# Optimization experiments

Measured on AMD Instinct MI355X. Metric: run time of the kernel, lower is better.

The kernel has to match this reference:

```python
import jax, jax.numpy as jnp
import numpy as np

B, GH, GW = 64, 14, 14
H = 512   # features_len == lstm hidden size == lstm_len
E = 512   # embedding_len
A = 512   # attention_len
V = 10000 # wordmap_len
MAXCAP = 50


def setup_inputs() -> dict:
    key = jax.random.key(0)
    ks = jax.random.split(key, 12)
    s = 0.02
    caplens = jax.random.randint(ks[2], (B, 1), 2, MAXCAP + 1, jnp.int32)
    caplens = caplens.at[0, 0].set(MAXCAP)  # ensure max(decode_lengths) == MAXCAP-1 (static T)
    return dict(
        image_features=jax.random.normal(ks[0], (B, GH, GW, H), jnp.float32),
        caps=jax.random.randint(ks[1], (B, MAXCAP), 0, V, jnp.int32),
        caplens=caplens,
        emb_table=jax.random.normal(ks[3], (V, E), jnp.float32) * s,
        W_ih=jax.random.normal(ks[4], (4 * H, E + H), jnp.float32) * s,
        W_hh=jax.random.normal(ks[5], (4 * H, H), jnp.float32) * s,
        b_ih=jnp.zeros((4 * H,), jnp.float32),
        b_hh=jnp.zeros((4 * H,), jnp.float32),
        W_enc=jax.random.normal(ks[6], (A, H), jnp.float32) * s,
        b_enc=jnp.zeros((A,), jnp.float32),
        W_dec=jax.random.normal(ks[7], (A, H), jnp.float32) * s,
        b_dec=jnp.zeros((A,), jnp.float32),
        W_full=jax.random.normal(ks[8], (1, A), jnp.float32) * s,
        b_full=jnp.zeros((1,), jnp.float32),
        W_score=jax.random.normal(ks[9], (V, H), jnp.float32) * s,
        b_score=jnp.zeros((V,), jnp.float32),
    )


def _forward(image_features, emb_table, W_ih, W_hh, b_ih, b_hh,
             W_enc, b_enc, W_dec, b_dec, W_full, b_full, W_score, b_score,
             caps, caplens):
    Bsz = image_features.shape[0]
    feats = image_features.reshape(Bsz, -1, image_features.shape[-1])  # (B, P, H)
    cl = caplens[:, 0]
    sort_ind = jnp.argsort(-cl)                      # descending sort by caption length
    cl = cl[sort_ind]
    feats = feats[sort_ind]
    caps_s = caps[sort_ind]
    decode_lengths = cl - 1
    T = caps.shape[1] - 1                            # static; setup guarantees max(decode_lengths)==T
    emb = emb_table[caps_s]                          # (B, MAXCAP, E)
    enc_att = jnp.einsum('bph,ah->bpa', feats, W_enc) + b_enc  # precomputed encoder attention proj
    mask = jnp.arange(T)[None, :] < decode_lengths[:, None]    # (B, T): row active at step t

    h0 = jnp.zeros((Bsz, feats.shape[-1]), feats.dtype)
    c0 = jnp.zeros_like(h0)

    def step(carry, xs):
        h, c = carry
        emb_t, m_t = xs                              # (B,E), (B,)
        # attention (show-attend-tell style)
        att2 = h @ W_dec.T + b_dec                   # (B, A)
        e = jnp.einsum('bpa,a->bp', jax.nn.relu(enc_att + att2[:, None, :]), W_full[0]) + b_full[0]
        alpha = jax.nn.softmax(e, axis=-1)           # (B, P)
        ctx = jnp.einsum('bp,bph->bh', alpha, feats) # (B, H)
        # LSTMCell
        x = jnp.concatenate([emb_t, ctx], axis=1)    # (B, E+H)
        gates = x @ W_ih.T + b_ih + h @ W_hh.T + b_hh
        i, f, g, o = jnp.split(gates, 4, axis=1)
        c_new = jax.nn.sigmoid(f) * c + jax.nn.sigmoid(i) * jnp.tanh(g)
        h_new = jax.nn.sigmoid(o) * jnp.tanh(c_new)
        score = h_new @ W_score.T + b_score          # (B, V)
        m = m_t[:, None]
        # rows past their decode length keep stale state and write zeros (matches :k slicing)
        h = jnp.where(m, h_new, h)
        c = jnp.where(m, c_new, c)
        return (h, c), (jnp.where(m, score, jnp.zeros((), score.dtype)),
                        jnp.where(m, alpha, jnp.zeros((), alpha.dtype)))

    (_, _), (scores, weights) = jax.lax.scan(
        step, (h0, c0), (emb[:, :T, :].transpose(1, 0, 2), mask.T))
    scores = scores.transpose(1, 0, 2)   # (B, T, V)
    weights = weights.transpose(1, 0, 2) # (B, T, P)
    return scores, caps_s, decode_lengths, weights, sort_ind


def reference(image_features, caps, caplens, emb_table, W_ih, W_hh, b_ih, b_hh,
              W_enc, b_enc, W_dec, b_dec, W_full, b_full, W_score, b_score):
    return _forward(image_features, emb_table, W_ih, W_hh, b_ih, b_hh,
                    W_enc, b_enc, W_dec, b_dec, W_full, b_full, W_score, b_score,
                    caps, caplens)
```

## Files before the change

kernel.cpp:

```cpp
#include <hip/hip_runtime.h>
#include <math.h>


#define WS_SORT   0
#define WS_DL     64
#define WS_NB     128
#define WS_ROWOFF 192
#define WS_CAPS   256
#define WS_RMAP   3456
#define WS_H      6592
#define WS_C      39360
#define WS_ATT2   72128
#define WS_E      104896
#define WS_Z      117696
#define WS_CTXP   117952
#define WS_PG     249024
#define WS_HALL   2346176
#define WS_ENC    3951808

#define OUT_SCORES 0
#define OUT_CAPS   31360000
#define OUT_DL     31363200
#define OUT_W      31363264
#define OUT_SORT   31977920

#define LSW 196

__device__ __forceinline__ float sigm(float x) { return 1.f / (1.f + expf(-x)); }

__device__ __forceinline__ float4 f4add(float4 a, float4 b) {
  return make_float4(a.x + b.x, a.y + b.y, a.z + b.z, a.w + b.w);
}

__device__ __forceinline__ int swz128(int m) { return (m >> 3) * 12 + (m & 7); }

__device__ __forceinline__ void stage128_strided(const float* __restrict__ src, int row0, int ld, int k0,
                                                 float* __restrict__ dst, int tid, int nrows_valid) {
#pragma unroll
  for (int i = 0; i < 2; ++i) {
    int lin = tid + 256 * i;
    int m = lin >> 2, kf = lin & 3;
    float4 v = make_float4(0.f, 0.f, 0.f, 0.f);
    if (m < nrows_valid) v = *(const float4*)(src + (long)(row0 + m) * ld + k0 + kf * 4);
    int mc = swz128(m);
    dst[(kf * 4 + 0) * LSW + mc] = v.x;
    dst[(kf * 4 + 1) * LSW + mc] = v.y;
    dst[(kf * 4 + 2) * LSW + mc] = v.z;
    dst[(kf * 4 + 3) * LSW + mc] = v.w;
  }
}

__device__ __forceinline__ void stage128_gather(const float* __restrict__ src, const int* __restrict__ bases,
                                                int k0, float* __restrict__ dst, int tid) {
#pragma unroll
  for (int i = 0; i < 2; ++i) {
    int lin = tid + 256 * i;
    int m = lin >> 2, kf = lin & 3;
    float4 v = *(const float4*)(src + bases[m] + k0 + kf * 4);
    int mc = swz128(m);
    dst[(kf * 4 + 0) * LSW + mc] = v.x;
    dst[(kf * 4 + 1) * LSW + mc] = v.y;
    dst[(kf * 4 + 2) * LSW + mc] = v.z;
    dst[(kf * 4 + 3) * LSW + mc] = v.w;
  }
}

__device__ __forceinline__ void gemm_acc128(const float* __restrict__ As, const float* __restrict__ Bs,
                                            float acc[8][8], int tx, int ty) {
#pragma unroll
  for (int kk = 0; kk < 16; ++kk) {
    const float4* ar = (const float4*)(As + kk * LSW + tx * 12);
    const float4* br = (const float4*)(Bs + kk * LSW + ty * 12);
    float4 a0 = ar[0], a1 = ar[1];
    float4 b0 = br[0], b1 = br[1];
    float av[8] = {a0.x, a0.y, a0.z, a0.w, a1.x, a1.y, a1.z, a1.w};
    float bv[8] = {b0.x, b0.y, b0.z, b0.w, b1.x, b1.y, b1.z, b1.w};
#pragma unroll
    for (int i = 0; i < 8; ++i)
#pragma unroll
      for (int j = 0; j < 8; ++j)
        acc[i][j] = fmaf(av[i], bv[j], acc[i][j]);
  }
}

__global__ __launch_bounds__(64) void setup_kernel(const int* __restrict__ caps, const int* __restrict__ caplens,
                                                   float* __restrict__ ws, float* __restrict__ out) {
  __shared__ int cl_s[64], so_s[64], dl_s[64], nb_s[49], ro_s[50];
  int i = threadIdx.x;
  cl_s[i] = caplens[i];
  __syncthreads();
  int cli = cl_s[i];
  int r = 0;
  for (int j = 0; j < 64; ++j) {
    int clj = cl_s[j];
    r += (clj > cli) || (clj == cli && j < i);
  }
  so_s[r] = i;
  dl_s[r] = cli - 1;
  __syncthreads();
  int* iws = (int*)ws;
  iws[WS_SORT + i] = so_s[i];
  iws[WS_DL + i] = dl_s[i];
  out[OUT_SORT + i] = (float)so_s[i];
  out[OUT_DL + i] = (float)dl_s[i];
  if (i < 49) {
    int n = 0;
    for (int b = 0; b < 64; ++b) n += (dl_s[b] > i);
    iws[WS_NB + i] = n;
    nb_s[i] = n;
  }
  __syncthreads();
  if (i == 0) {
    int acc = 0;
    for (int t = 0; t < 49; ++t) { ro_s[t] = acc; acc += nb_s[t]; }
    ro_s[49] = acc;
    iws[WS_NB + 49] = acc;
  }
  __syncthreads();
  if (i < 50) iws[WS_ROWOFF + i] = ro_s[i];
  int R = ro_s[49];
  for (int rr = i; rr < 3136; rr += 64) {
    int val = 0;
    if (rr < R) {
      int t = 0;
      while (t < 48 && ro_s[t + 1] <= rr) ++t;
      val = t * 64 + (rr - ro_s[t]);
    }
    iws[WS_RMAP + rr] = val;
  }
  for (int j = i; j < 3200; j += 64) {
    int k = j / 50, jj = j - k * 50;
    int cv = caps[so_s[k] * 50 + jj];
    iws[WS_CAPS + j] = cv;
    out[OUT_CAPS + j] = (float)cv;
  }
}

__global__ void zero_init_kernel(float* __restrict__ out, float* __restrict__ ws, const float* __restrict__ b_dec) {
  const float4 z = make_float4(0.f, 0.f, 0.f, 0.f);
  float4* out4 = (float4*)out;
  float4* ws4 = (float4*)ws;
  const float4* bd4 = (const float4*)b_dec;
  for (long idx = (long)blockIdx.x * 256 + threadIdx.x; idx < 8018240L; idx += (long)gridDim.x * 256) {
    if (idx < 7840000L) {
      out4[idx] = z;
    } else if (idx < 7993664L) {
      out4[7840816L + (idx - 7840000L)] = z;
    } else if (idx < 8010048L) {
      ws4[1648L + (idx - 7993664L)] = z;
    } else {
      long j = idx - 8010048L;
      ws4[18032L + j] = bd4[j & 127];
    }
  }
}

__global__ __launch_bounds__(256) void encatt_kernel(const float* __restrict__ image, const float* __restrict__ W_enc,
                                                     const float* __restrict__ b_enc, float* __restrict__ ws) {
  __shared__ __align__(16) float As[16 * LSW];
  __shared__ __align__(16) float Bs[16 * LSW];
  __shared__ int rb[128];
  int tid = threadIdx.x;
  const int* iws = (const int*)ws;
  int mt = blockIdx.x, nt = blockIdx.y;
  if (tid < 128) {
    int r = mt * 128 + tid;
    int b = r / 196;
    int p = r - b * 196;
    rb[tid] = iws[WS_SORT + b] * 100352 + p * 512;
  }
  float acc[8][8] = {};
  for (int ch = 0; ch < 32; ++ch) {
    __syncthreads();
    stage128_gather(image, rb, ch * 16, As, tid);
    stage128_strided(W_enc, nt * 128, 512, ch * 16, Bs, tid, 128);
    __syncthreads();
    gemm_acc128(As, Bs, acc, tid & 15, tid >> 4);
  }
  int tx = tid & 15, ty = tid >> 4;
  int r0 = mt * 128 + tx * 8;
  int n0 = nt * 128 + ty * 8;
#pragma unroll
  for (int i = 0; i < 8; ++i) {
    float* cp = ws + WS_ENC + (long)(r0 + i) * 512 + n0;
    *(float4*)(cp)     = make_float4(acc[i][0] + b_enc[n0],     acc[i][1] + b_enc[n0 + 1],
                                     acc[i][2] + b_enc[n0 + 2], acc[i][3] + b_enc[n0 + 3]);
    *(float4*)(cp + 4) = make_float4(acc[i][4] + b_enc[n0 + 4], acc[i][5] + b_enc[n0 + 5],
                                     acc[i][6] + b_enc[n0 + 6], acc[i][7] + b_enc[n0 + 7]);
  }
}

__global__ __launch_bounds__(512) void ectx_kernel(float* __restrict__ ws, const float* __restrict__ image,
                                                   const float* __restrict__ W_full, const float* __restrict__ b_full,
                                                   int t) {
  const int* iws = (const int*)ws;
  int b = blockIdx.x;
  if (b >= iws[WS_NB + t]) return;
  int pg = blockIdx.y;
  __shared__ float att2_s[512], wf_s[512], e_s[52];
  int tid = threadIdx.x;
  att2_s[tid] = ws[WS_ATT2 + b * 512 + tid];
  wf_s[tid] = W_full[tid];
  __syncthreads();
  int w = tid >> 6, lane = tid & 63;
  float bf0 = b_full[0];
  for (int idx = w; idx < 49; idx += 8) {
    int p = pg * 49 + idx;
    const float* er = ws + WS_ENC + (long)(b * 196 + p) * 512;
    float acc = 0.f;
#pragma unroll
    for (int a8 = 0; a8 < 8; ++a8) {
      int a = (a8 << 6) + lane;
      float v = er[a] + att2_s[a];
      acc = fmaf(fmaxf(v, 0.f), wf_s[a], acc);
    }
#pragma unroll
    for (int off = 32; off; off >>= 1) acc += __shfl_down(acc, off);
    if (lane == 0) e_s[idx] = expf(acc + bf0);
  }
  __syncthreads();
  if (tid < 49) ws[WS_E + b * 200 + pg * 49 + tid] = e_s[tid];
  if (tid == 0) {
    float zz = 0.f;
    for (int j = 0; j < 49; ++j) zz += e_s[j];
    ws[WS_Z + pg * 64 + b] = zz;
  }
  long sb = (long)iws[WS_SORT + b] * 100352;
  float a0 = 0.f;
  for (int j = 0; j < 49; ++j) {
    a0 = fmaf(e_s[j], image[sb + (long)(pg * 49 + j) * 512 + tid], a0);
  }
  ws[WS_CTXP + pg * 32768 + b * 512 + tid] = a0;
}

__global__ __launch_bounds__(256) void gates_kernel(float* __restrict__ ws, const float* __restrict__ emb,
                                                    const float* __restrict__ W_ih, const float* __restrict__ W_hh,
                                                    int t) {
  __shared__ __align__(16) float As[96 * 68];
  __shared__ __align__(16) float Bs[96 * 68];
  __shared__ int rbe[64];
  __shared__ float rcpz_s[64];
  int tid = threadIdx.x;
  int nt = blockIdx.x;
  int ks = blockIdx.y;
  int* iws = (int*)ws;
  if (tid < 64) {
    rbe[tid] = iws[WS_CAPS + tid * 50 + t] * 512;
    float zz = ws[WS_Z + tid] + ws[WS_Z + 64 + tid] + ws[WS_Z + 128 + tid] + ws[WS_Z + 192 + tid];
    rcpz_s[tid] = 1.f / zz;
  }
  __syncthreads();
#pragma unroll
  for (int c = 0; c < 3; ++c) {
    int k0 = ks * 96 + c * 32;
#pragma unroll
    for (int i = 0; i < 2; ++i) {
      int lin = tid + 256 * i;
      int kf = lin >> 6;
      int m = lin & 63;
      float4 v;
      if (k0 < 512) {
        v = *(const float4*)(emb + (long)rbe[m] + k0 + kf * 4);
      } else if (k0 < 1024) {
        const float* base = ws + WS_CTXP + m * 512 + (k0 - 512) + kf * 4;
        float4 v0 = *(const float4*)(base);
        float4 v1 = *(const float4*)(base + 32768);
        float4 v2 = *(const float4*)(base + 65536);
        float4 v3 = *(const float4*)(base + 98304);
        float rz = rcpz_s[m];
        v = make_float4((v0.x + v1.x + v2.x + v3.x) * rz, (v0.y + v1.y + v2.y + v3.y) * rz,
                        (v0.z + v1.z + v2.z + v3.z) * rz, (v0.w + v1.w + v2.w + v3.w) * rz);
      } else {
        v = *(const float4*)(ws + WS_H + m * 512 + (k0 - 1024) + kf * 4);
      }
      float* da = As + (c * 32 + kf * 4) * 68 + m;
      da[0] = v.x; da[68] = v.y; da[136] = v.z; da[204] = v.w;
      const float* srcB = (k0 < 1024) ? (W_ih + (long)(nt * 64 + m) * 1024 + k0 + kf * 4)
                                      : (W_hh + (long)(nt * 64 + m) * 512 + (k0 - 1024) + kf * 4);
      float4 bv = *(const float4*)srcB;
      float* db = Bs + (c * 32 + kf * 4) * 68 + m;
      db[0] = bv.x; db[68] = bv.y; db[136] = bv.z; db[204] = bv.w;
    }
  }
  __syncthreads();
  int w = tid >> 6, lane = tid & 63;
  int tx = lane & 7, ty = lane >> 3;
  float acc[8][2] = {};
#pragma unroll 8
  for (int kk = 0; kk < 96; ++kk) {
    const float4* ar = (const float4*)(As + kk * 68 + tx * 8);
    float4 a0 = ar[0], a1 = ar[1];
    float2 bv = *(const float2*)(Bs + kk * 68 + w * 16 + ty * 2);
    float av[8] = {a0.x, a0.y, a0.z, a0.w, a1.x, a1.y, a1.z, a1.w};
#pragma unroll
    for (int i = 0; i < 8; ++i) {
      acc[i][0] = fmaf(av[i], bv.x, acc[i][0]);
      acc[i][1] = fmaf(av[i], bv.y, acc[i][1]);
    }
  }
  float* pg = ws + WS_PG + ks * 131072;
  int j0 = nt * 64 + w * 16 + ty * 2;
#pragma unroll
  for (int i = 0; i < 8; ++i) {
    int b = tx * 8 + i;
    *(float2*)(pg + b * 2048 + j0) = make_float2(acc[i][0], acc[i][1]);
  }
}

__global__ __launch_bounds__(512) void lstm_att2_kernel(float* __restrict__ ws, const float* __restrict__ b_ih,
                                                        const float* __restrict__ b_hh, const float* __restrict__ W_dec,
                                                        const float* __restrict__ b_dec, float* __restrict__ out, int t) {
  const int* iws = (const int*)ws;
  int b = blockIdx.x;
  int as = blockIdx.y;
  int hh = threadIdx.x;
  int nb = iws[WS_NB + t];
  __shared__ float h_s[512], red[512];
  float gi = b_ih[hh] + b_hh[hh];
  float gf = b_ih[512 + hh] + b_hh[512 + hh];
  float gg = b_ih[1024 + hh] + b_hh[1024 + hh];
  float go = b_ih[1536 + hh] + b_hh[1536 + hh];
  const float* pgp = ws + WS_PG + b * 2048;
#pragma unroll
  for (int ks = 0; ks < 16; ++ks) {
    const float* p = pgp + ks * 131072;
    gi += p[hh]; gf += p[512 + hh]; gg += p[1024 + hh]; go += p[1536 + hh];
  }
  float c = ws[WS_C + b * 512 + hh];
  float cn = sigm(gf) * c + sigm(gi) * tanhf(gg);
  float hn = sigm(go) * tanhf(cn);
  h_s[hh] = hn;
  if (b < nb) {
    if (as == 0) {
      ws[WS_C + b * 512 + hh] = cn;
      ws[WS_H + b * 512 + hh] = hn;
      ws[WS_HALL + (long)(iws[WS_ROWOFF + t] + b) * 512 + hh] = hn;
    }
    if (hh < 49) {
      float zz = ws[WS_Z + b] + ws[WS_Z + 64 + b] + ws[WS_Z + 128 + b] + ws[WS_Z + 192 + b];
      int p = as * 49 + hh;
      out[OUT_W + (long)(b * 49 + t) * 196 + p] = ws[WS_E + b * 200 + p] / zz;
    }
  }
  __syncthreads();
  int a = as * 128 + (hh >> 2);
  int part = hh & 3;
  const float* wd = W_dec + (long)a * 512 + part * 128;
  const float* hp = h_s + part * 128;
  float s = 0.f;
#pragma unroll 8
  for (int j = 0; j < 32; ++j) {
    float4 wv = *(const float4*)(wd + 4 * j);
    s = fmaf(hp[4 * j], wv.x, s);
    s = fmaf(hp[4 * j + 1], wv.y, s);
    s = fmaf(hp[4 * j + 2], wv.z, s);
    s = fmaf(hp[4 * j + 3], wv.w, s);
  }
  red[hh] = s;
  __syncthreads();
  if (part == 0) {
    float v = red[hh] + red[hh + 1] + red[hh + 2] + red[hh + 3] + b_dec[a];
    ws[WS_ATT2 + b * 512 + a] = v;
  }
}

__global__ __launch_bounds__(256) void score_kernel(const float* __restrict__ ws, const float* __restrict__ W_score,
                                                    const float* __restrict__ b_score, float* __restrict__ out) {
  __shared__ __align__(16) float As[16 * LSW];
  __shared__ __align__(16) float Bs[16 * LSW];
  const int* iws = (const int*)ws;
  int mt = blockIdx.x, nt = blockIdx.y;
  int R = iws[WS_NB + 49];
  if (mt * 128 >= R) return;
  int tid = threadIdx.x;
  int mvalid = R - mt * 128; if (mvalid > 128) mvalid = 128;
  int nvalid = 10000 - nt * 128; if (nvalid > 128) nvalid = 128;
  float acc[8][8] = {};
  for (int ch = 0; ch < 32; ++ch) {
    __syncthreads();
    stage128_strided(ws + WS_HALL, mt * 128, 512, ch * 16, As, tid, mvalid);
    stage128_strided(W_score, nt * 128, 512, ch * 16, Bs, tid, nvalid);
    __syncthreads();
    gemm_acc128(As, Bs, acc, tid & 15, tid >> 4);
  }
  int tx = tid & 15, ty = tid >> 4;
  int n0 = nt * 128 + ty * 8;
#pragma unroll
  for (int i = 0; i < 8; ++i) {
    int r = mt * 128 + tx * 8 + i;
    if (r >= R) continue;
    int tb = iws[WS_RMAP + r];
    int bb = tb & 63, tt = tb >> 6;
    float* cp = out + (long)bb * 490000 + tt * 10000 + n0;
    if (n0 + 4 <= 10000)
      *(float4*)(cp)     = make_float4(acc[i][0] + b_score[n0],     acc[i][1] + b_score[n0 + 1],
                                       acc[i][2] + b_score[n0 + 2], acc[i][3] + b_score[n0 + 3]);
    if (n0 + 8 <= 10000)
      *(float4*)(cp + 4) = make_float4(acc[i][4] + b_score[n0 + 4], acc[i][5] + b_score[n0 + 5],
                                       acc[i][6] + b_score[n0 + 6], acc[i][7] + b_score[n0 + 7]);
  }
}

extern "C" void kernel_launch(void* const* d_in, const int* in_sizes, int n_in,
                              void* d_out, int out_size, void* d_ws, size_t ws_size,
                              hipStream_t stream) {
  const float* image   = (const float*)d_in[0];
  const int*   caps    = (const int*)d_in[1];
  const int*   caplens = (const int*)d_in[2];
  const float* emb     = (const float*)d_in[3];
  const float* W_ih    = (const float*)d_in[4];
  const float* W_hh    = (const float*)d_in[5];
  const float* b_ih    = (const float*)d_in[6];
  const float* b_hh    = (const float*)d_in[7];
  const float* W_enc   = (const float*)d_in[8];
  const float* b_enc   = (const float*)d_in[9];
  const float* W_dec   = (const float*)d_in[10];
  const float* b_dec   = (const float*)d_in[11];
  const float* W_full  = (const float*)d_in[12];
  const float* b_full  = (const float*)d_in[13];
  const float* W_score = (const float*)d_in[14];
  const float* b_score = (const float*)d_in[15];
  float* out = (float*)d_out;
  float* ws  = (float*)d_ws;

  setup_kernel<<<1, 64, 0, stream>>>(caps, caplens, ws, out);
  zero_init_kernel<<<2048, 256, 0, stream>>>(out, ws, b_dec);
  encatt_kernel<<<dim3(98, 4), 256, 0, stream>>>(image, W_enc, b_enc, ws);
  for (int t = 0; t < 49; ++t) {
    ectx_kernel<<<dim3(64, 4), 512, 0, stream>>>(ws, image, W_full, b_full, t);
    gates_kernel<<<dim3(32, 16), 256, 0, stream>>>(ws, emb, W_ih, W_hh, t);
    lstm_att2_kernel<<<dim3(64, 4), 512, 0, stream>>>(ws, b_ih, b_hh, W_dec, b_dec, out, t);
  }
  score_kernel<<<dim3(25, 79), 256, 0, stream>>>(ws, W_score, b_score, out);
}
```

Baseline: 2.378 ms.

## Compute score GEMM on MFMA with split-bf16 hi/lo emulation of fp32

Replaces the fp32 SIMT score GEMM with bf16 MFMA instructions. Each fp32 operand is split into high and low bf16 halves and three products are accumulated to approximate fp32 accuracy. The LSTM kernel now stores hidden states in this packed form, and a new pre-pass packs W_score into workspace on every call. The cost is three MFMAs per tile, an extra pass over W_score, and scattered scalar output stores in place of float4 stores.

After: 2.307 ms. 2.9% less time.

```diff
diff --git a/kernel.cpp b/kernel.cpp
--- a/kernel.cpp
+++ b/kernel.cpp
@@ -26,10 +26,21 @@
 
 #define LSW 196
 
+typedef __attribute__((ext_vector_type(8))) short bf16x8;
+typedef __attribute__((ext_vector_type(4))) float f32x4;
+
 __device__ __forceinline__ float sigm(float x) { return 1.f / (1.f + expf(-x)); }
 
-__device__ __forceinline__ float4 f4add(float4 a, float4 b) {
-  return make_float4(a.x + b.x, a.y + b.y, a.z + b.z, a.w + b.w);
+__device__ __forceinline__ unsigned bf16_hi_bits(float x) {
+  unsigned u = __float_as_uint(x);
+  return (u + 0x7fffu + ((u >> 16) & 1u)) & 0xffff0000u;
+}
+__device__ __forceinline__ unsigned pack_bf16x2(float x) {
+  unsigned hb = bf16_hi_bits(x);
+  float lo = x - __uint_as_float(hb);
+  unsigned u = __float_as_uint(lo);
+  unsigned lb = ((u + 0x7fffu + ((u >> 16) & 1u)) >> 16) & 0xffffu;
+  return hb | lb;
 }
 
 __device__ __forceinline__ int swz128(int m) { return (m >> 3) * 12 + (m & 7); }
@@ -334,7 +345,7 @@
     if (as == 0) {
       ws[WS_C + b * 512 + hh] = cn;
       ws[WS_H + b * 512 + hh] = hn;
-      ws[WS_HALL + (long)(iws[WS_ROWOFF + t] + b) * 512 + hh] = hn;
+      ((unsigned*)ws)[WS_HALL + (long)(iws[WS_ROWOFF + t] + b) * 512 + hh] = pack_bf16x2(hn);
     }
     if (hh < 49) {
       float zz = ws[WS_Z + b] + ws[WS_Z + 64 + b] + ws[WS_Z + 128 + b] + ws[WS_Z + 192 + b];
@@ -364,40 +375,94 @@
   }
 }
 
-__global__ __launch_bounds__(256) void score_kernel(const float* __restrict__ ws, const float* __restrict__ W_score,
+__global__ void pack_wscore_kernel(const float* __restrict__ W_score, float* __restrict__ ws) {
+  unsigned* dst = (unsigned*)(ws + WS_ENC);
+  for (int idx = blockIdx.x * 256 + threadIdx.x; idx < 5120000; idx += gridDim.x * 256) {
+    dst[idx] = pack_bf16x2(W_score[idx]);
+  }
+}
+
+__global__ __launch_bounds__(256) void score_kernel(const float* __restrict__ ws,
                                                     const float* __restrict__ b_score, float* __restrict__ out) {
-  __shared__ __align__(16) float As[16 * LSW];
-  __shared__ __align__(16) float Bs[16 * LSW];
+  __shared__ ushort Ah[8192], Al[8192], Bh[8192], Bl[8192];
   const int* iws = (const int*)ws;
+  int R = iws[WS_NB + 49];
   int mt = blockIdx.x, nt = blockIdx.y;
-  int R = iws[WS_NB + 49];
   if (mt * 128 >= R) return;
   int tid = threadIdx.x;
-  int mvalid = R - mt * 128; if (mvalid > 128) mvalid = 128;
-  int nvalid = 10000 - nt * 128; if (nvalid > 128) nvalid = 128;
-  float acc[8][8] = {};
-  for (int ch = 0; ch < 32; ++ch) {
+  int w = tid >> 6, lane = tid & 63;
+  int g = lane >> 4, lm = lane & 15;
+  const unsigned* Au = (const unsigned*)(ws + WS_HALL);
+  const unsigned* Bu = (const unsigned*)(ws + WS_ENC);
+  f32x4 acc[8][2] = {};
+  for (int kc = 0; kc < 8; ++kc) {
+    int k0 = kc * 64;
     __syncthreads();
-    stage128_strided(ws + WS_HALL, mt * 128, 512, ch * 16, As, tid, mvalid);
-    stage128_strided(W_score, nt * 128, 512, ch * 16, Bs, tid, nvalid);
+#pragma unroll
+    for (int i = 0; i < 8; ++i) {
+      int idx = tid + 256 * i;
+      int row = idx >> 4, c4 = (idx & 15) * 4;
+      int off = (row * 128 + c4 * 2) ^ ((row & 7) << 4);
+      uint4 va = make_uint4(0u, 0u, 0u, 0u);
+      int ar = mt * 128 + row;
+      if (ar < R) va = *(const uint4*)(Au + (long)ar * 512 + k0 + c4);
+      *(ushort4*)((char*)Ah + off) = make_ushort4((ushort)(va.x >> 16), (ushort)(va.y >> 16),
+                                                  (ushort)(va.z >> 16), (ushort)(va.w >> 16));
+      *(ushort4*)((char*)Al + off) = make_ushort4((ushort)(va.x & 0xffff), (ushort)(va.y & 0xffff),
+                                                  (ushort)(va.z & 0xffff), (ushort)(va.w & 0xffff));
+      uint4 vb = make_uint4(0u, 0u, 0u, 0u);
+      int br = nt * 128 + row;
+      if (br < 10000) vb = *(const uint4*)(Bu + (long)br * 512 + k0 + c4);
+      *(ushort4*)((char*)Bh + off) = make_ushort4((ushort)(vb.x >> 16), (ushort)(vb.y >> 16),
+                                                  (ushort)(vb.z >> 16), (ushort)(vb.w >> 16));
+      *(ushort4*)((char*)Bl + off) = make_ushort4((ushort)(vb.x & 0xffff), (ushort)(vb.y & 0xffff),
+                                                  (ushort)(vb.z & 0xffff), (ushort)(vb.w & 0xffff));
+    }
     __syncthreads();
-    gemm_acc128(As, Bs, acc, tid & 15, tid >> 4);
-  }
-  int tx = tid & 15, ty = tid >> 4;
-  int n0 = nt * 128 + ty * 8;
-#pragma unroll
-  for (int i = 0; i < 8; ++i) {
-    int r = mt * 128 + tx * 8 + i;
-    if (r >= R) continue;
-    int tb = iws[WS_RMAP + r];
-    int bb = tb & 63, tt = tb >> 6;
-    float* cp = out + (long)bb * 490000 + tt * 10000 + n0;
-    if (n0 + 4 <= 10000)
-      *(float4*)(cp)     = make_float4(acc[i][0] + b_score[n0],     acc[i][1] + b_score[n0 + 1],
-                                       acc[i][2] + b_score[n0 + 2], acc[i][3] + b_score[n0 + 3]);
-    if (n0 + 8 <= 10000)
-      *(float4*)(cp + 4) = make_float4(acc[i][4] + b_score[n0 + 4], acc[i][5] + b_score[n0 + 5],
-                                       acc[i][6] + b_score[n0 + 6], acc[i][7] + b_score[n0 + 7]);
+#pragma unroll
+    for (int ks2 = 0; ks2 < 2; ++ks2) {
+      int kb = ks2 * 64 + g * 16;
+      bf16x8 bhf0, bhf1, blf0, blf1;
+      {
+        int rn0 = w * 32 + lm;
+        int off0 = (rn0 * 128 + kb) ^ ((rn0 & 7) << 4);
+        bhf0 = *(const bf16x8*)((const char*)Bh + off0);
+        blf0 = *(const bf16x8*)((const char*)Bl + off0);
+        int rn1 = w * 32 + 16 + lm;
+        int off1 = (rn1 * 128 + kb) ^ ((rn1 & 7) << 4);
+        bhf1 = *(const bf16x8*)((const char*)Bh + off1);
+        blf1 = *(const bf16x8*)((const char*)Bl + off1);
+      }
+#pragma unroll
+      for (int mf = 0; mf < 8; ++mf) {
+        int rm = mf * 16 + lm;
+        int off = (rm * 128 + kb) ^ ((rm & 7) << 4);
+        bf16x8 ah = *(const bf16x8*)((const char*)Ah + off);
+        bf16x8 al = *(const bf16x8*)((const char*)Al + off);
+        acc[mf][0] = __builtin_amdgcn_mfma_f32_16x16x32_bf16(ah, bhf0, acc[mf][0], 0, 0, 0);
+        acc[mf][0] = __builtin_amdgcn_mfma_f32_16x16x32_bf16(ah, blf0, acc[mf][0], 0, 0, 0);
+        acc[mf][0] = __builtin_amdgcn_mfma_f32_16x16x32_bf16(al, bhf0, acc[mf][0], 0, 0, 0);
+        acc[mf][1] = __builtin_amdgcn_mfma_f32_16x16x32_bf16(ah, bhf1, acc[mf][1], 0, 0, 0);
+        acc[mf][1] = __builtin_amdgcn_mfma_f32_16x16x32_bf16(ah, blf1, acc[mf][1], 0, 0, 0);
+        acc[mf][1] = __builtin_amdgcn_mfma_f32_16x16x32_bf16(al, bhf1, acc[mf][1], 0, 0, 0);
+      }
+    }
+  }
+#pragma unroll
+  for (int mf = 0; mf < 8; ++mf) {
+#pragma unroll
+    for (int r = 0; r < 4; ++r) {
+      int grow = mt * 128 + mf * 16 + g * 4 + r;
+      if (grow >= R) continue;
+      int tb = iws[WS_RMAP + grow];
+      int bb = tb & 63, tt = tb >> 6;
+      float* cp = out + (long)bb * 490000 + tt * 10000;
+#pragma unroll
+      for (int nf = 0; nf < 2; ++nf) {
+        int n = nt * 128 + w * 32 + nf * 16 + lm;
+        if (n < 10000) cp[n] = acc[mf][nf][r] + b_score[n];
+      }
+    }
   }
 }
 
@@ -431,5 +496,6 @@
     gates_kernel<<<dim3(32, 16), 256, 0, stream>>>(ws, emb, W_ih, W_hh, t);
     lstm_att2_kernel<<<dim3(64, 4), 512, 0, stream>>>(ws, b_ih, b_hh, W_dec, b_dec, out, t);
   }
-  score_kernel<<<dim3(25, 79), 256, 0, stream>>>(ws, W_score, b_score, out);
-}
+  pack_wscore_kernel<<<2048, 256, 0, stream>>>(W_score, ws);
+  score_kernel<<<dim3(25, 79), 256, 0, stream>>>(ws, b_score, out);
+}
```
